# Optimization experiments

Measured on AMD Instinct MI355X. Metric: run time of the kernel, lower is better.

Reference implementation:

```python
import jax, jax.numpy as jnp
import numpy as np

EPS = 1e-10


def setup_inputs() -> dict:
    key = jax.random.key(0)
    k1, k2 = jax.random.split(key)
    inputs = jax.random.normal(k1, (32, 64, 64, 64), dtype=jnp.float32)
    # tf.random_uniform_initializer() default: U(-0.05, 0.05)
    embeddings = jax.random.uniform(k2, (1024, 64), dtype=jnp.float32,
                                    minval=-0.05, maxval=0.05)
    return {"inputs": inputs, "embeddings": embeddings}


def reference(inputs, embeddings):
    beta = 0.25
    K, D = embeddings.shape
    input_shape = inputs.shape
    flat = inputs.reshape(-1, D)                      # [N, D]

    # squared L2 distances: |a|^2 - 2 a.b + |b|^2  -> [N, K]
    a_sq = jnp.sum(flat * flat, axis=1, keepdims=True)
    ab = 2.0 * (flat @ embeddings.T)
    b_sq = jnp.sum(embeddings * embeddings, axis=1)[None, :]
    distances = a_sq - ab + b_sq

    idx = jnp.argmin(distances, axis=1)               # [N]
    # gather nearest codes (equivalent to one_hot @ embeddings)
    quantized = embeddings[idx].reshape(input_shape)

    commitment_loss = jnp.mean(jnp.square(jax.lax.stop_gradient(quantized) - inputs))
    codebook_loss = jnp.mean(jnp.square(quantized - jax.lax.stop_gradient(inputs)))
    vq_loss = commitment_loss + beta * codebook_loss

    # straight-through estimator
    quantized_st = inputs + jax.lax.stop_gradient(quantized - inputs)

    # perplexity from code usage histogram (== mean of one-hot rows)
    N = flat.shape[0]
    counts = jnp.zeros((K,), dtype=jnp.float32).at[idx].add(1.0)
    avg_probs = counts / N
    perplexity = jnp.exp(-jnp.sum(avg_probs * jnp.log(avg_probs + EPS)))

    indices_reshaped = idx.reshape(input_shape[:-1])
    return quantized_st, indices_reshaped, perplexity, vq_loss
```

## Files before the change

### kernel.cpp

```cpp
#include <hip/hip_runtime.h>
#include <float.h>

#define N_ROWS 131072
#define DIM 64
#define KCODES 1024
#define TAU_HALF 5.0e-4f
#define NBLOCKA (N_ROWS / 128)
#define NPART (NBLOCKA * 4)

typedef __attribute__((ext_vector_type(8))) short short8;
typedef __attribute__((ext_vector_type(4))) float f32x4;

__device__ __forceinline__ unsigned short f2bf_rne(float x) {
    unsigned int u = __float_as_uint(x);
    unsigned int r = u + 0x7FFFu + ((u >> 16) & 1u);
    return (unsigned short)(r >> 16);
}
__device__ __forceinline__ float bf2f(unsigned short h) {
    return __uint_as_float(((unsigned int)h) << 16);
}

__device__ __forceinline__ float np_pairwise_sq64(const float* v) {
    float r[8];
#pragma unroll
    for (int j = 0; j < 8; ++j) r[j] = __fmul_rn(v[j], v[j]);
#pragma unroll
    for (int i = 8; i < 64; i += 8)
#pragma unroll
        for (int j = 0; j < 8; ++j)
            r[j] = __fadd_rn(r[j], __fmul_rn(v[i + j], v[i + j]));
    return __fadd_rn(
        __fadd_rn(__fadd_rn(r[0], r[1]), __fadd_rn(r[2], r[3])),
        __fadd_rn(__fadd_rn(r[4], r[5]), __fadd_rn(r[6], r[7])));
}

__device__ __forceinline__ float np_sq_stream(const float* xr) {
    float r[8];
    {
        float4 a = *reinterpret_cast<const float4*>(xr);
        float4 b = *reinterpret_cast<const float4*>(xr + 4);
        r[0] = __fmul_rn(a.x, a.x); r[1] = __fmul_rn(a.y, a.y);
        r[2] = __fmul_rn(a.z, a.z); r[3] = __fmul_rn(a.w, a.w);
        r[4] = __fmul_rn(b.x, b.x); r[5] = __fmul_rn(b.y, b.y);
        r[6] = __fmul_rn(b.z, b.z); r[7] = __fmul_rn(b.w, b.w);
    }
#pragma unroll
    for (int i = 8; i < 64; i += 8) {
        float4 a = *reinterpret_cast<const float4*>(xr + i);
        float4 b = *reinterpret_cast<const float4*>(xr + i + 4);
        r[0] = __fadd_rn(r[0], __fmul_rn(a.x, a.x));
        r[1] = __fadd_rn(r[1], __fmul_rn(a.y, a.y));
        r[2] = __fadd_rn(r[2], __fmul_rn(a.z, a.z));
        r[3] = __fadd_rn(r[3], __fmul_rn(a.w, a.w));
        r[4] = __fadd_rn(r[4], __fmul_rn(b.x, b.x));
        r[5] = __fadd_rn(r[5], __fmul_rn(b.y, b.y));
        r[6] = __fadd_rn(r[6], __fmul_rn(b.z, b.z));
        r[7] = __fadd_rn(r[7], __fmul_rn(b.w, b.w));
    }
    return __fadd_rn(
        __fadd_rn(__fadd_rn(r[0], r[1]), __fadd_rn(r[2], r[3])),
        __fadd_rn(__fadd_rn(r[4], r[5]), __fadd_rn(r[6], r[7])));
}

__device__ __forceinline__ float np_dist_stream(const float* xr, const float* e,
                                                float a_sq, float bq) {
    double acc0 = 0.0, acc1 = 0.0, acc2 = 0.0, acc3 = 0.0;
#pragma unroll
    for (int d = 0; d < DIM; d += 4) {
        float4 ev = *reinterpret_cast<const float4*>(e + d);
        float4 xv = *reinterpret_cast<const float4*>(xr + d);
        acc0 = fma((double)xv.x, (double)ev.x, acc0);
        acc1 = fma((double)xv.y, (double)ev.y, acc1);
        acc2 = fma((double)xv.z, (double)ev.z, acc2);
        acc3 = fma((double)xv.w, (double)ev.w, acc3);
    }
    double dot = (acc0 + acc1) + (acc2 + acc3);
    float ab = (float)(2.0 * dot);
    return __fadd_rn(__fsub_rn(a_sq, ab), bq);
}

__global__ __launch_bounds__(256, 4)
void vq_prep(const float* __restrict__ emb,
             int* __restrict__ hist,
             float* __restrict__ bsqf,
             unsigned short* __restrict__ epack) {
    const int tid = blockIdx.x * 256 + threadIdx.x;
    const int c   = tid >> 4;
    const int sub = tid & 15;
    const int g   = sub & 7;
    const int lvl = sub >> 3;

    const float* e8 = emb + (size_t)c * DIM + g * 8;
    float4 v0 = *reinterpret_cast<const float4*>(e8);
    float4 v1 = *reinterpret_cast<const float4*>(e8 + 4);
    float ev[8] = {v0.x, v0.y, v0.z, v0.w, v1.x, v1.y, v1.z, v1.w};
    short8 outv;
#pragma unroll
    for (int j = 0; j < 8; ++j) {
        unsigned short hh = f2bf_rne(ev[j]);
        outv[j] = (lvl == 0) ? (short)hh : (short)f2bf_rne(ev[j] - bf2f(hh));
    }
    const size_t base =
        ((((size_t)(c >> 4) * 2 + lvl) * 2 + (g >> 2)) * 64 +
         (((g & 3) << 4) | (c & 15))) * 8;
    *reinterpret_cast<short8*>(epack + base) = outv;

    if (sub == 0) {
        float e[DIM];
        const float4* src = reinterpret_cast<const float4*>(emb + (size_t)c * DIM);
#pragma unroll
        for (int i = 0; i < DIM / 4; ++i) {
            float4 v = src[i];
            e[i * 4 + 0] = v.x; e[i * 4 + 1] = v.y;
            e[i * 4 + 2] = v.z; e[i * 4 + 3] = v.w;
        }
        bsqf[c] = np_pairwise_sq64(e);
        hist[c] = 0;
    }
}

__global__ __launch_bounds__(256, 4)
void vq_fast(const float* __restrict__ x,
             const float* __restrict__ emb,
             const unsigned short* __restrict__ epack,
             const float* __restrict__ bsqf,
             float* __restrict__ idxout,
             float* __restrict__ qout,
             int* __restrict__ hist,
             float* __restrict__ partials) {
    __shared__ unsigned short lds[16384];
    __shared__ float bql[KCODES];
    __shared__ float aql[4][2][16];

    const int t = threadIdx.x;
    const int lane = t & 63;
    const int wid = t >> 6;
    const int rowbase = blockIdx.x * 128 + wid * 32;
    const int arow = lane & 15;
    const int kgrp = lane >> 4;

#pragma unroll
    for (int i = 0; i < 4; ++i) bql[t + i * 256] = bsqf[t + i * 256];

    short8 ah[2][2], al[2][2];
#pragma unroll
    for (int mf = 0; mf < 2; ++mf) {
        float ssq = 0.f;
#pragma unroll
        for (int kt = 0; kt < 2; ++kt) {
            const float* src = x + (size_t)(rowbase + mf * 16 + arow) * DIM + kt * 32 + kgrp * 8;
            float4 v0 = *reinterpret_cast<const float4*>(src);
            float4 v1 = *reinterpret_cast<const float4*>(src + 4);
            float xv[8] = {v0.x, v0.y, v0.z, v0.w, v1.x, v1.y, v1.z, v1.w};
            short8 h, l;
#pragma unroll
            for (int j = 0; j < 8; ++j) {
                unsigned short hh = f2bf_rne(xv[j]);
                h[j] = (short)hh;
                l[j] = (short)f2bf_rne(xv[j] - bf2f(hh));
                ssq = fmaf(xv[j], xv[j], ssq);
            }
            ah[mf][kt] = h;
            al[mf][kt] = l;
        }
        ssq += __shfl_xor(ssq, 16);
        ssq += __shfl_xor(ssq, 32);
        if (kgrp == 0) aql[wid][mf][arow] = ssq;
    }

    float best[2][4], sec[2][4];
    int bidx[2][4], sidx[2][4];
#pragma unroll
    for (int mf = 0; mf < 2; ++mf)
#pragma unroll
        for (int r = 0; r < 4; ++r) {
            best[mf][r] = -FLT_MAX; sec[mf][r] = -FLT_MAX;
            bidx[mf][r] = 0; sidx[mf][r] = 0;
        }

    for (int ch = 0; ch < 8; ++ch) {
        __syncthreads();
        {
            const float4* gsrc = reinterpret_cast<const float4*>(epack + (size_t)ch * 16384);
            float4* ldst = reinterpret_cast<float4*>(lds);
#pragma unroll
            for (int i = 0; i < 8; ++i)
                ldst[t + i * 256] = gsrc[t + i * 256];
        }
        __syncthreads();

        for (int ctl = 0; ctl < 8; ++ctl) {
            const int code0 = (ch * 8 + ctl) * 16;
            const unsigned short* fb = lds + ctl * 2048 + lane * 8;
            short8 bh0 = *reinterpret_cast<const short8*>(fb + 0 * 512);
            short8 bh1 = *reinterpret_cast<const short8*>(fb + 1 * 512);
            short8 bl0 = *reinterpret_cast<const short8*>(fb + 2 * 512);
            short8 bl1 = *reinterpret_cast<const short8*>(fb + 3 * 512);
            const float nb = -0.5f * bql[code0 + arow];

            f32x4 acc[2];
#pragma unroll
            for (int mf = 0; mf < 2; ++mf) {
                f32x4 a = {nb, nb, nb, nb};
                a = __builtin_amdgcn_mfma_f32_16x16x32_bf16(ah[mf][0], bh0, a, 0, 0, 0);
                a = __builtin_amdgcn_mfma_f32_16x16x32_bf16(ah[mf][1], bh1, a, 0, 0, 0);
                a = __builtin_amdgcn_mfma_f32_16x16x32_bf16(ah[mf][0], bl0, a, 0, 0, 0);
                a = __builtin_amdgcn_mfma_f32_16x16x32_bf16(ah[mf][1], bl1, a, 0, 0, 0);
                a = __builtin_amdgcn_mfma_f32_16x16x32_bf16(al[mf][0], bh0, a, 0, 0, 0);
                a = __builtin_amdgcn_mfma_f32_16x16x32_bf16(al[mf][1], bh1, a, 0, 0, 0);
                acc[mf] = a;
            }

            const int code = code0 + arow;
#pragma unroll
            for (int mf = 0; mf < 2; ++mf)
#pragma unroll
                for (int r = 0; r < 4; ++r) {
                    float m = acc[mf][r];
                    bool gt_b = m > best[mf][r];
                    bool gt_s = m > sec[mf][r];
                    sec[mf][r]  = gt_b ? best[mf][r] : (gt_s ? m : sec[mf][r]);
                    sidx[mf][r] = gt_b ? bidx[mf][r] : (gt_s ? code : sidx[mf][r]);
                    best[mf][r] = gt_b ? m : best[mf][r];
                    bidx[mf][r] = gt_b ? code : bidx[mf][r];
                }
        }
    }

#pragma unroll
    for (int mf = 0; mf < 2; ++mf)
#pragma unroll
        for (int r = 0; r < 4; ++r) {
            float b = best[mf][r], sc = sec[mf][r];
            int bi = bidx[mf][r], si = sidx[mf][r];
#pragma unroll
            for (int off = 1; off < 16; off <<= 1) {
                float ob  = __shfl_xor(b, off);
                int   obi = __shfl_xor(bi, off);
                float osc = __shfl_xor(sc, off);
                int   osi = __shfl_xor(si, off);
                bool o_gt = ob > b;
                float loser  = o_gt ? b  : ob;
                int   loseri = o_gt ? bi : obi;
                b  = o_gt ? ob  : b;
                bi = o_gt ? obi : bi;
                float ns = sc; int nsi = si;
                if (osc > ns)   { ns = osc;   nsi = osi; }
                if (loser > ns) { ns = loser; nsi = loseri; }
                sc = ns; si = nsi;
            }
            best[mf][r] = b; sec[mf][r] = sc;
            bidx[mf][r] = bi; sidx[mf][r] = si;
        }

    __syncthreads();
    int* ldsK = reinterpret_cast<int*>(lds);

    if ((lane & 15) == 0) {
        const int rgrp = lane >> 4;
        float lsum = 0.f;
#pragma unroll
        for (int mf = 0; mf < 2; ++mf)
#pragma unroll
            for (int r = 0; r < 4; ++r) {
                int rl = rgrp * 4 + r;
                int rloc = wid * 32 + mf * 16 + rl;
                int bi = bidx[mf][r], si = sidx[mf][r];
                int k = bi;
                if (best[mf][r] - sec[mf][r] <= TAU_HALF) {
                    int c1 = min(bi, si), c2 = max(bi, si);
                    const float* xr = x + (size_t)(rowbase - wid * 32 + rloc) * DIM;
                    float a_sq = np_sq_stream(xr);
                    float d1 = np_dist_stream(xr, emb + (size_t)c1 * DIM, a_sq, bql[c1]);
                    float d2 = np_dist_stream(xr, emb + (size_t)c2 * DIM, a_sq, bql[c2]);
                    k = (d2 < d1) ? c2 : c1;
                }
                ldsK[rloc] = k;
                lsum += fmaf(-2.0f, best[mf][r], aql[wid][mf][rl]);
            }
        lsum += __shfl_xor(lsum, 16);
        lsum += __shfl_xor(lsum, 32);
        if (lane == 0) partials[blockIdx.x * 4 + wid] = lsum;
    }
    __syncthreads();

    const int blkrow0 = blockIdx.x * 128;
#pragma unroll
    for (int i = 0; i < 8; ++i) {
        int seg_row = wid * 32 + i * 4 + (lane >> 4);
        int k = ldsK[seg_row];
        const float4* er = reinterpret_cast<const float4*>(emb + (size_t)k * DIM) + (lane & 15);
        float4* qr = reinterpret_cast<float4*>(qout + (size_t)(blkrow0 + seg_row) * DIM) + (lane & 15);
        *qr = *er;
    }
    if (t < 128) {
        int k = ldsK[t];
        idxout[blkrow0 + t] = (float)k;
        atomicAdd(&hist[k], 1);
    }
}

__global__ void vq_final(const int* __restrict__ hist,
                         const float* __restrict__ partials,
                         float* __restrict__ out2) {
    __shared__ double sh[KCODES];
    __shared__ double sl[KCODES];
    int t = threadIdx.x;

    double p = (double)hist[t] * (1.0 / (double)N_ROWS);
    sh[t] = p * log(p + 1e-10);

    double ls = 0.0;
#pragma unroll
    for (int i = 0; i < NPART / KCODES; ++i)
        ls += (double)partials[t + i * KCODES];
    sl[t] = ls;
    __syncthreads();

    for (int off = KCODES / 2; off > 0; off >>= 1) {
        if (t < off) { sh[t] += sh[t + off]; sl[t] += sl[t + off]; }
        __syncthreads();
    }
    if (t == 0) {
        out2[0] = (float)exp(-sh[0]);
        out2[1] = (float)(1.25 * sl[0] * (1.0 / (double)((size_t)N_ROWS * DIM)));
    }
}

extern "C" void kernel_launch(void* const* d_in, const int* in_sizes, int n_in,
                              void* d_out, int out_size, void* d_ws, size_t ws_size,
                              hipStream_t stream) {
    const float* x   = (const float*)d_in[0];
    const float* emb = (const float*)d_in[1];
    float* out = (float*)d_out;

    int*   hist      = (int*)d_ws;
    float* bsqf      = (float*)((char*)d_ws + 4096);
    float* partials  = (float*)((char*)d_ws + 8192);
    unsigned short* epack = (unsigned short*)((char*)d_ws + 40960);

    float* qout    = out;
    float* idxout  = out + 8388608;
    float* scalars = out + 8388608 + 131072;

    vq_prep <<<64, 256, 0, stream>>>(emb, hist, bsqf, epack);
    vq_fast <<<NBLOCKA, 256, 0, stream>>>(x, emb, epack, bsqf, idxout, qout,
                                          hist, partials);
    vq_final<<<1, KCODES, 0, stream>>>(hist, partials, scalars);
}
```

Measured before the change: 103.4 us.

## Move histogram from global atomics into final kernel LDS and use nontemporal stores

Removes the per-row global atomicAdd on the code histogram from the main kernel. Instead the single-block final kernel re-reads the written index output and builds the histogram with shared-memory atomics. The quantized output copy now uses nontemporal stores to avoid polluting cache. The trade-off is that one 1024-thread block must now serially read 131072 indices, which lengthens the tail kernel.

Result: slower. 132.7 us (+28.3%).

```diff
diff --git a/kernel.cpp b/kernel.cpp
--- a/kernel.cpp
+++ b/kernel.cpp
@@ -81,7 +81,6 @@
 
 __global__ __launch_bounds__(256, 4)
 void vq_prep(const float* __restrict__ emb,
-             int* __restrict__ hist,
              float* __restrict__ bsqf,
              unsigned short* __restrict__ epack) {
     const int tid = blockIdx.x * 256 + threadIdx.x;
@@ -115,7 +114,6 @@
             e[i * 4 + 2] = v.z; e[i * 4 + 3] = v.w;
         }
         bsqf[c] = np_pairwise_sq64(e);
-        hist[c] = 0;
     }
 }
 
@@ -126,7 +124,6 @@
              const float* __restrict__ bsqf,
              float* __restrict__ idxout,
              float* __restrict__ qout,
-             int* __restrict__ hist,
              float* __restrict__ partials) {
     __shared__ unsigned short lds[16384];
     __shared__ float bql[KCODES];
@@ -289,25 +286,37 @@
     for (int i = 0; i < 8; ++i) {
         int seg_row = wid * 32 + i * 4 + (lane >> 4);
         int k = ldsK[seg_row];
-        const float4* er = reinterpret_cast<const float4*>(emb + (size_t)k * DIM) + (lane & 15);
-        float4* qr = reinterpret_cast<float4*>(qout + (size_t)(blkrow0 + seg_row) * DIM) + (lane & 15);
-        *qr = *er;
+        const f32x4* er = reinterpret_cast<const f32x4*>(emb + (size_t)k * DIM) + (lane & 15);
+        f32x4* qr = reinterpret_cast<f32x4*>(qout + (size_t)(blkrow0 + seg_row) * DIM) + (lane & 15);
+        f32x4 v = *er;
+        __builtin_nontemporal_store(v, qr);
     }
     if (t < 128) {
         int k = ldsK[t];
         idxout[blkrow0 + t] = (float)k;
-        atomicAdd(&hist[k], 1);
-    }
-}
-
-__global__ void vq_final(const int* __restrict__ hist,
-                         const float* __restrict__ partials,
-                         float* __restrict__ out2) {
+    }
+}
+
+__global__ __launch_bounds__(1024, 1)
+void vq_final(const float* __restrict__ idxout,
+              const float* __restrict__ partials,
+              float* __restrict__ out2) {
+    __shared__ int shist[KCODES];
     __shared__ double sh[KCODES];
     __shared__ double sl[KCODES];
-    int t = threadIdx.x;
-
-    double p = (double)hist[t] * (1.0 / (double)N_ROWS);
+    const int t = threadIdx.x;
+
+    shist[t] = 0;
+    __syncthreads();
+
+#pragma unroll 4
+    for (int i = 0; i < N_ROWS / 1024; ++i) {
+        int k = (int)idxout[t + i * 1024];
+        atomicAdd(&shist[k], 1);
+    }
+    __syncthreads();
+
+    double p = (double)shist[t] * (1.0 / (double)N_ROWS);
     sh[t] = p * log(p + 1e-10);
 
     double ls = 0.0;
@@ -334,17 +343,16 @@
     const float* emb = (const float*)d_in[1];
     float* out = (float*)d_out;
 
-    int*   hist      = (int*)d_ws;
-    float* bsqf      = (float*)((char*)d_ws + 4096);
-    float* partials  = (float*)((char*)d_ws + 8192);
-    unsigned short* epack = (unsigned short*)((char*)d_ws + 40960);
+    float* bsqf      = (float*)d_ws;
+    float* partials  = (float*)((char*)d_ws + 4096);
+    unsigned short* epack = (unsigned short*)((char*)d_ws + 36864);
 
     float* qout    = out;
     float* idxout  = out + 8388608;
     float* scalars = out + 8388608 + 131072;
 
-    vq_prep <<<64, 256, 0, stream>>>(emb, hist, bsqf, epack);
+    vq_prep <<<64, 256, 0, stream>>>(emb, bsqf, epack);
     vq_fast <<<NBLOCKA, 256, 0, stream>>>(x, emb, epack, bsqf, idxout, qout,
-                                          hist, partials);
-    vq_final<<<1, KCODES, 0, stream>>>(hist, partials, scalars);
-}
+                                          partials);
+    vq_final<<<1, 1024, 0, stream>>>(idxout, partials, scalars);
+}
```
